# Performance work log

Hardware: AMD Instinct MI355X
Metric: run time of the kernel (lower is better)

The kernel has to match this reference:

```python
import jax, jax.numpy as jnp
import numpy as np

N_NODES = 100000
N_EDGES = 3200000
N_ELEMS = 10


def setup_inputs() -> dict:
    key = jax.random.key(0)
    k1, k2, k3, k4, k5 = jax.random.split(key, 5)
    # edge distances in (0.1, 5.1) Angstrom, shape [E, 1]
    x = jax.random.uniform(k1, (N_EDGES, 1), dtype=jnp.float32) * 5.0 + 0.1
    # one-hot-ish node element encoding; only argmax matters
    node_attrs = jax.random.normal(k2, (N_NODES, N_ELEMS), dtype=jnp.float32)
    edge_index = jax.random.randint(k3, (2, N_EDGES), 0, N_NODES)
    # atomic numbers of the chemical species present (1..89)
    atomic_numbers = jax.random.randint(k4, (N_ELEMS,), 1, 90)
    # stand-in for ase.data.covalent_radii (119 entries, ~0.3..2.3 A)
    covalent_radii = jax.random.uniform(k5, (119,), dtype=jnp.float32) * 2.0 + 0.3
    return {
        "x": x,
        "node_attrs": node_attrs,
        "edge_index": edge_index,
        "atomic_numbers": atomic_numbers,
        "covalent_radii": covalent_radii,
    }


def _polynomial_envelope(x, r_max, p):
    # PolynomialCutoff.calculate_envelope, p = 6
    r = x / r_max
    env = (1.0
           - (p + 1.0) * (p + 2.0) / 2.0 * jnp.power(r, p)
           + p * (p + 2.0) * jnp.power(r, p + 1)
           - p * (p + 1.0) / 2.0 * jnp.power(r, p + 2))
    return env * (x < r_max)


def reference(x, node_attrs, edge_index, atomic_numbers, covalent_radii):
    c = jnp.array([0.1818, 0.5099, 0.2802, 0.02817], dtype=jnp.float32)
    p = 6.0
    a_exp = jnp.float32(0.3)
    a_prefactor = jnp.float32(0.4543)

    sender, receiver = edge_index[0], edge_index[1]
    # per-node atomic number from one-hot attrs, [N, 1]
    node_Z = atomic_numbers[jnp.argmax(node_attrs, axis=1)][..., None]
    Z_u = node_Z[sender].astype(jnp.int32)  # [E, 1]
    Z_v = node_Z[receiver].astype(jnp.int32)  # [E, 1]
    Zu_f = Z_u.astype(jnp.float32)
    Zv_f = Z_v.astype(jnp.float32)

    a = a_prefactor * 0.529 / (jnp.power(Zu_f, a_exp) + jnp.power(Zv_f, a_exp))
    r_over_a = x / a  # [E, 1]
    phi = (c[0] * jnp.exp(-3.2 * r_over_a)
           + c[1] * jnp.exp(-0.9423 * r_over_a)
           + c[2] * jnp.exp(-0.4028 * r_over_a)
           + c[3] * jnp.exp(-0.2016 * r_over_a))
    v_edges = 14.3996 * Zu_f * Zv_f / x * phi  # [E, 1]

    r_max = covalent_radii[Z_u] + covalent_radii[Z_v]  # [E, 1]
    envelope = _polynomial_envelope(x, r_max, p)
    v_edges = 0.5 * v_edges * envelope  # [E, 1]

    # scatter-sum edge energies into receiver nodes -> [N]
    V_ZBL = jax.ops.segment_sum(v_edges[:, 0], receiver,
                                num_segments=node_attrs.shape[0])
    return V_ZBL
```

## Files before the change

### kernel.cpp

```cpp
#include <hip/hip_runtime.h>
#include <stdint.h>

#define N_NODES 100000
#define N_ELEM4 50000
#define N_EDGES 3200000
#define N_ELEMS 10
#define N_PAIRS (N_ELEMS * N_ELEMS)

#define NB 256
#define NPB 391
#define SCAT_THREADS 1024
#define NBLK 512
#define EPB 6256
#define NGROUPS (EPB / 4)
#define NG4 (N_EDGES / 4)
#define PREP_BLOCKS 196
#define CAP 16384

__global__ __launch_bounds__(256) void prep_kernel(
    const float* __restrict__ node_attrs,
    const int* __restrict__ atomic_numbers,
    const float* __restrict__ covalent_radii,
    uint8_t* __restrict__ node_elem4,
    float4* __restrict__ pair_tab,
    unsigned int* __restrict__ g_cnt) {
  int i = blockIdx.x * 256 + threadIdx.x;

  if (blockIdx.x == 0) {
    if (threadIdx.x < N_PAIRS) {
      int t = threadIdx.x;
      int eu = t / N_ELEMS, ev = t % N_ELEMS;
      float Zuf = (float)atomic_numbers[eu];
      float Zvf = (float)atomic_numbers[ev];
      float a = 0.4543f * 0.529f / (powf(Zuf, 0.3f) + powf(Zvf, 0.3f));
      float rmax = covalent_radii[(int)Zuf] + covalent_radii[(int)Zvf];
      pair_tab[t] = make_float4(1.0f / a, 0.5f * 14.3996f * Zuf * Zvf,
                                rmax, 1.0f / rmax);
    }
    if (threadIdx.x < NB) g_cnt[threadIdx.x] = 0u;
  }

  if (i < N_ELEM4) {
    unsigned int packed = 0;
#pragma unroll
    for (int h = 0; h < 2; ++h) {
      int node = 2 * i + h;
      const float2* row = (const float2*)(node_attrs + (size_t)node * N_ELEMS);
      float best = -INFINITY;
      int bj = 0;
#pragma unroll
      for (int k = 0; k < 5; ++k) {
        float2 v = row[k];
        if (v.x > best) { best = v.x; bj = 2 * k; }
        if (v.y > best) { best = v.y; bj = 2 * k + 1; }
      }
      packed |= (unsigned int)bj << (h * 4);
    }
    node_elem4[i] = (uint8_t)packed;
  }
}

__device__ __forceinline__ float edge_val(float xi, int u, int v,
                                          const uint8_t* s_elem4,
                                          const float4* s_tab) {
  int eu = (s_elem4[u >> 1] >> ((u & 1) * 4)) & 0xF;
  int ev = (s_elem4[v >> 1] >> ((v & 1) * 4)) & 0xF;
  float4 tb = s_tab[eu * N_ELEMS + ev];
  float roa = xi * tb.x;
  float phi = 0.1818f  * __expf(-3.2f    * roa)
            + 0.5099f  * __expf(-0.9423f * roa)
            + 0.2802f  * __expf(-0.4028f * roa)
            + 0.02817f * __expf(-0.2016f * roa);
  float val = tb.y * phi * __builtin_amdgcn_rcpf(xi);
  float r  = xi * tb.w;
  float r2 = r * r;
  float r6 = r2 * r2 * r2;
  float env = 1.0f - 28.0f * r6 + 48.0f * r6 * r - 21.0f * r6 * r2;
  return (xi < tb.z) ? val * env : 0.0f;
}

__global__ __launch_bounds__(SCAT_THREADS, 8) void scatter_kernel(
    const float* __restrict__ x,
    const int* __restrict__ edge_index,
    const uint8_t* __restrict__ node_elem4,
    const float4* __restrict__ pair_tab,
    unsigned int* __restrict__ g_cnt,
    unsigned int* __restrict__ records) {
  __shared__ uint4        s_elem4_v[N_ELEM4 / 16];
  __shared__ float4       s_tab[N_PAIRS];
  __shared__ unsigned int s_cnt[NB];
  __shared__ unsigned int s_goff[NB];
  const uint8_t* s_elem4 = (const uint8_t*)s_elem4_v;

  int tid = threadIdx.x;

  {
    const uint4* src = (const uint4*)node_elem4;
    for (int j = tid; j < N_ELEM4 / 16; j += SCAT_THREADS) s_elem4_v[j] = src[j];
  }
  if (tid < N_PAIRS) s_tab[tid] = pair_tab[tid];
  if (tid < NB) s_cnt[tid] = 0u;
  __syncthreads();

  float val[8];
  unsigned int pk[8];

#pragma unroll
  for (int k = 0; k < 2; ++k) {
    int gl = k * SCAT_THREADS + tid;
    int g  = blockIdx.x * NGROUPS + gl;
    bool ok = (gl < NGROUPS) && (g < NG4);
    int e = g * 4;
    float4 xv = make_float4(1, 1, 1, 1);
    int4 uu = make_int4(0, 0, 0, 0), vv = make_int4(0, 0, 0, 0);
    if (ok) {
      xv = *(const float4*)(x + e);
      uu = *(const int4*)(edge_index + e);
      vv = *(const int4*)(edge_index + N_EDGES + e);
    }
    int rv[4] = {vv.x, vv.y, vv.z, vv.w};
    int ru[4] = {uu.x, uu.y, uu.z, uu.w};
    float xs[4] = {xv.x, xv.y, xv.z, xv.w};
#pragma unroll
    for (int c = 0; c < 4; ++c) {
      int j = k * 4 + c;
      pk[j] = 0xFFFFFFFFu;
      if (ok) {
        float v = edge_val(xs[c], ru[c], rv[c], s_elem4, s_tab);
        if (v != 0.0f) {
          unsigned int b = (unsigned int)rv[c] / NPB;
          unsigned int lid = (unsigned int)rv[c] - b * NPB;
          unsigned int r = atomicAdd(&s_cnt[b], 1u);
          pk[j] = (b << 22) | (r << 9) | lid;
          val[j] = v;
        }
      }
    }
  }
  __syncthreads();

  if (tid < NB) s_goff[tid] = atomicAdd(&g_cnt[tid], s_cnt[tid]);
  __syncthreads();

#pragma unroll
  for (int j = 0; j < 8; ++j) {
    if (pk[j] != 0xFFFFFFFFu) {
      unsigned int b = pk[j] >> 22;
      unsigned int r = (pk[j] >> 9) & 0x1FFFu;
      records[((size_t)b << 14) + s_goff[b] + r] =
          (__float_as_uint(val[j]) & ~0x1FFu) | (pk[j] & 0x1FFu);
    }
  }
}

__global__ __launch_bounds__(1024) void reduce_kernel(
    const unsigned int* __restrict__ g_cnt,
    const unsigned int* __restrict__ records,
    float* __restrict__ out) {
  __shared__ float bins[NPB];
  int b = blockIdx.x, tid = threadIdx.x;

  if (tid < NPB) bins[tid] = 0.0f;
  __syncthreads();

  unsigned int cnt = g_cnt[b];
  const unsigned int* rp = records + ((size_t)b << 14);
  for (unsigned int i = tid; i < cnt; i += 1024) {
    unsigned int rec = rp[i];
    atomicAdd(&bins[rec & 0x1FFu], __uint_as_float(rec & ~0x1FFu));
  }
  __syncthreads();

  int nb0 = b * NPB;
  if (tid < NPB && nb0 + tid < N_NODES) out[nb0 + tid] = bins[tid];
}

extern "C" void kernel_launch(void* const* d_in, const int* in_sizes, int n_in,
                              void* d_out, int out_size, void* d_ws, size_t ws_size,
                              hipStream_t stream) {
  const float* x              = (const float*)d_in[0];
  const float* node_attrs     = (const float*)d_in[1];
  const int*   edge_index     = (const int*)d_in[2];
  const int*   atomic_numbers = (const int*)d_in[3];
  const float* covalent_radii = (const float*)d_in[4];
  float* out = (float*)d_out;

  char* wsp = (char*)d_ws;
  unsigned int* records    = (unsigned int*)wsp;
  unsigned int* g_cnt      = (unsigned int*)(wsp + 16777216);
  float4*       pair_tab   = (float4*)(wsp + 16778240);
  uint8_t*      node_elem4 = (uint8_t*)(wsp + 16779840);

  prep_kernel<<<PREP_BLOCKS, 256, 0, stream>>>(
      node_attrs, atomic_numbers, covalent_radii, node_elem4, pair_tab, g_cnt);

  scatter_kernel<<<NBLK, SCAT_THREADS, 0, stream>>>(
      x, edge_index, node_elem4, pair_tab, g_cnt, records);

  reduce_kernel<<<NB, 1024, 0, stream>>>(g_cnt, records, out);
}
```

Before: 111.6 us.

## Replace bucketed record scatter and reduce pass with direct global atomics

Drops the two-phase scheme, which bucketed edge energies into per-bin record arrays in workspace and summed them in a separate reduce kernel. Each nonzero edge value is now added straight into the output with a global float atomicAdd, and the prep kernel zeroes the output first. This removes the 12.8MB record write and read-back plus one kernel launch, but adds up to 3.2M contended global atomics on random addresses and makes the summation order nondeterministic.

```diff
diff --git a/kernel.cpp b/kernel.cpp
--- a/kernel.cpp
+++ b/kernel.cpp
@@ -7,15 +7,12 @@
 #define N_ELEMS 10
 #define N_PAIRS (N_ELEMS * N_ELEMS)
 
-#define NB 256
-#define NPB 391
 #define SCAT_THREADS 1024
 #define NBLK 512
 #define EPB 6256
 #define NGROUPS (EPB / 4)
 #define NG4 (N_EDGES / 4)
 #define PREP_BLOCKS 196
-#define CAP 16384
 
 __global__ __launch_bounds__(256) void prep_kernel(
     const float* __restrict__ node_attrs,
@@ -23,22 +20,21 @@
     const float* __restrict__ covalent_radii,
     uint8_t* __restrict__ node_elem4,
     float4* __restrict__ pair_tab,
-    unsigned int* __restrict__ g_cnt) {
+    float4* __restrict__ out4) {
   int i = blockIdx.x * 256 + threadIdx.x;
 
-  if (blockIdx.x == 0) {
-    if (threadIdx.x < N_PAIRS) {
-      int t = threadIdx.x;
-      int eu = t / N_ELEMS, ev = t % N_ELEMS;
-      float Zuf = (float)atomic_numbers[eu];
-      float Zvf = (float)atomic_numbers[ev];
-      float a = 0.4543f * 0.529f / (powf(Zuf, 0.3f) + powf(Zvf, 0.3f));
-      float rmax = covalent_radii[(int)Zuf] + covalent_radii[(int)Zvf];
-      pair_tab[t] = make_float4(1.0f / a, 0.5f * 14.3996f * Zuf * Zvf,
-                                rmax, 1.0f / rmax);
-    }
-    if (threadIdx.x < NB) g_cnt[threadIdx.x] = 0u;
+  if (blockIdx.x == 0 && threadIdx.x < N_PAIRS) {
+    int t = threadIdx.x;
+    int eu = t / N_ELEMS, ev = t % N_ELEMS;
+    float Zuf = (float)atomic_numbers[eu];
+    float Zvf = (float)atomic_numbers[ev];
+    float a = 0.4543f * 0.529f / (powf(Zuf, 0.3f) + powf(Zvf, 0.3f));
+    float rmax = covalent_radii[(int)Zuf] + covalent_radii[(int)Zvf];
+    pair_tab[t] = make_float4(1.0f / a, 0.5f * 14.3996f * Zuf * Zvf,
+                              rmax, 1.0f / rmax);
   }
+
+  if (i < N_NODES / 4) out4[i] = make_float4(0.f, 0.f, 0.f, 0.f);
 
   if (i < N_ELEM4) {
     unsigned int packed = 0;
@@ -79,17 +75,14 @@
   return (xi < tb.z) ? val * env : 0.0f;
 }
 
-__global__ __launch_bounds__(SCAT_THREADS, 8) void scatter_kernel(
+__global__ __launch_bounds__(SCAT_THREADS) void scatter_kernel(
     const float* __restrict__ x,
     const int* __restrict__ edge_index,
     const uint8_t* __restrict__ node_elem4,
     const float4* __restrict__ pair_tab,
-    unsigned int* __restrict__ g_cnt,
-    unsigned int* __restrict__ records) {
-  __shared__ uint4        s_elem4_v[N_ELEM4 / 16];
-  __shared__ float4       s_tab[N_PAIRS];
-  __shared__ unsigned int s_cnt[NB];
-  __shared__ unsigned int s_goff[NB];
+    float* __restrict__ out) {
+  __shared__ uint4  s_elem4_v[N_ELEM4 / 16];
+  __shared__ float4 s_tab[N_PAIRS];
   const uint8_t* s_elem4 = (const uint8_t*)s_elem4_v;
 
   int tid = threadIdx.x;
@@ -99,80 +92,27 @@
     for (int j = tid; j < N_ELEM4 / 16; j += SCAT_THREADS) s_elem4_v[j] = src[j];
   }
   if (tid < N_PAIRS) s_tab[tid] = pair_tab[tid];
-  if (tid < NB) s_cnt[tid] = 0u;
   __syncthreads();
-
-  float val[8];
-  unsigned int pk[8];
 
 #pragma unroll
   for (int k = 0; k < 2; ++k) {
     int gl = k * SCAT_THREADS + tid;
     int g  = blockIdx.x * NGROUPS + gl;
-    bool ok = (gl < NGROUPS) && (g < NG4);
+    if (gl >= NGROUPS || g >= NG4) continue;
     int e = g * 4;
-    float4 xv = make_float4(1, 1, 1, 1);
-    int4 uu = make_int4(0, 0, 0, 0), vv = make_int4(0, 0, 0, 0);
-    if (ok) {
-      xv = *(const float4*)(x + e);
-      uu = *(const int4*)(edge_index + e);
-      vv = *(const int4*)(edge_index + N_EDGES + e);
-    }
+    float4 xv = *(const float4*)(x + e);
+    int4 uu = *(const int4*)(edge_index + e);
+    int4 vv = *(const int4*)(edge_index + N_EDGES + e);
+    int ru[4] = {uu.x, uu.y, uu.z, uu.w};
     int rv[4] = {vv.x, vv.y, vv.z, vv.w};
-    int ru[4] = {uu.x, uu.y, uu.z, uu.w};
     float xs[4] = {xv.x, xv.y, xv.z, xv.w};
 #pragma unroll
     for (int c = 0; c < 4; ++c) {
-      int j = k * 4 + c;
-      pk[j] = 0xFFFFFFFFu;
-      if (ok) {
-        float v = edge_val(xs[c], ru[c], rv[c], s_elem4, s_tab);
-        if (v != 0.0f) {
-          unsigned int b = (unsigned int)rv[c] / NPB;
-          unsigned int lid = (unsigned int)rv[c] - b * NPB;
-          unsigned int r = atomicAdd(&s_cnt[b], 1u);
-          pk[j] = (b << 22) | (r << 9) | lid;
-          val[j] = v;
-        }
-      }
+      float v = edge_val(xs[c], ru[c], rv[c], s_elem4, s_tab);
+      if (v != 0.0f)
+        atomicAdd(&out[rv[c]], v);
     }
   }
-  __syncthreads();
-
-  if (tid < NB) s_goff[tid] = atomicAdd(&g_cnt[tid], s_cnt[tid]);
-  __syncthreads();
-
-#pragma unroll
-  for (int j = 0; j < 8; ++j) {
-    if (pk[j] != 0xFFFFFFFFu) {
-      unsigned int b = pk[j] >> 22;
-      unsigned int r = (pk[j] >> 9) & 0x1FFFu;
-      records[((size_t)b << 14) + s_goff[b] + r] =
-          (__float_as_uint(val[j]) & ~0x1FFu) | (pk[j] & 0x1FFu);
-    }
-  }
-}
-
-__global__ __launch_bounds__(1024) void reduce_kernel(
-    const unsigned int* __restrict__ g_cnt,
-    const unsigned int* __restrict__ records,
-    float* __restrict__ out) {
-  __shared__ float bins[NPB];
-  int b = blockIdx.x, tid = threadIdx.x;
-
-  if (tid < NPB) bins[tid] = 0.0f;
-  __syncthreads();
-
-  unsigned int cnt = g_cnt[b];
-  const unsigned int* rp = records + ((size_t)b << 14);
-  for (unsigned int i = tid; i < cnt; i += 1024) {
-    unsigned int rec = rp[i];
-    atomicAdd(&bins[rec & 0x1FFu], __uint_as_float(rec & ~0x1FFu));
-  }
-  __syncthreads();
-
-  int nb0 = b * NPB;
-  if (tid < NPB && nb0 + tid < N_NODES) out[nb0 + tid] = bins[tid];
 }
 
 extern "C" void kernel_launch(void* const* d_in, const int* in_sizes, int n_in,
@@ -186,16 +126,13 @@
   float* out = (float*)d_out;
 
   char* wsp = (char*)d_ws;
-  unsigned int* records    = (unsigned int*)wsp;
-  unsigned int* g_cnt      = (unsigned int*)(wsp + 16777216);
-  float4*       pair_tab   = (float4*)(wsp + 16778240);
-  uint8_t*      node_elem4 = (uint8_t*)(wsp + 16779840);
+  float4*  pair_tab   = (float4*)wsp;
+  uint8_t* node_elem4 = (uint8_t*)(wsp + 1600);
 
   prep_kernel<<<PREP_BLOCKS, 256, 0, stream>>>(
-      node_attrs, atomic_numbers, covalent_radii, node_elem4, pair_tab, g_cnt);
+      node_attrs, atomic_numbers, covalent_radii, node_elem4, pair_tab,
+      (float4*)out);
 
   scatter_kernel<<<NBLK, SCAT_THREADS, 0, stream>>>(
-      x, edge_index, node_elem4, pair_tab, g_cnt, records);
-
-  reduce_kernel<<<NB, 1024, 0, stream>>>(g_cnt, records, out);
+      x, edge_index, node_elem4, pair_tab, out);
 }
```

Result: slower. 159.1 us (+42.6%).
